# Kernel tuning notes

Hardware: AMD Instinct MI355X
Metric: run time of the kernel (lower is better)

Reference implementation:

```python
import jax, jax.numpy as jnp
import numpy as np

B, NQ, HW, C, H = 4, 1024, 4096, 1024, 8
DH = C // H  # 128


def setup_inputs() -> dict:
    key = jax.random.key(0)
    ks = jax.random.split(key, 11)
    s = 0.02
    return {
        "query": jax.random.normal(ks[0], (B, NQ, C), dtype=jnp.float32),
        "memory": jax.random.normal(ks[1], (B, HW, C), dtype=jnp.float32),
        "mask": jax.random.uniform(ks[2], (B, NQ, HW), dtype=jnp.float32),
        "Wq": jax.random.normal(ks[3], (C, C), dtype=jnp.float32) * s,
        "bq": jnp.zeros((C,), dtype=jnp.float32),
        "Wk": jax.random.normal(ks[4], (C, C), dtype=jnp.float32) * s,
        "bk": jnp.zeros((C,), dtype=jnp.float32),
        "Wv": jax.random.normal(ks[5], (C, C), dtype=jnp.float32) * s,
        "bv": jnp.zeros((C,), dtype=jnp.float32),
        "Wo": jax.random.normal(ks[6], (C, C), dtype=jnp.float32) * s,
        "bo": jnp.zeros((C,), dtype=jnp.float32),
    }


def reference(query, memory, mask, Wq, bq, Wk, bk, Wv, bv, Wo, bo):
    # Projections (torch nn.Linear convention: x @ W.T + b)
    q = (query @ Wq.T + bq).reshape(B, NQ, H, DH)
    k = (memory @ Wk.T + bk).reshape(B, HW, H, DH)
    v = (memory @ Wv.T + bv).reshape(B, HW, H, DH)

    scale = 1.0 / jnp.sqrt(jnp.asarray(DH, dtype=q.dtype))
    scores = jnp.einsum("bqhd,bkhd->bhqk", q * scale, k)  # [B,H,NQ,HW]

    # mask < 0.5 means disallowed (True in torch bool attn_mask -> -inf)
    allowed = (mask >= 0.5)[:, None, :, :]  # broadcast over heads
    scores = jnp.where(allowed, scores, jnp.asarray(-jnp.inf, dtype=scores.dtype))

    attn = jax.nn.softmax(scores, axis=-1)
    out = jnp.einsum("bhqk,bkhd->bqhd", attn, v).reshape(B, NQ, C)
    return out @ Wo.T + bo
```

## Files before the change

### kernel.cpp

```cpp
#include <hip/hip_runtime.h>


#define NB 4
#define NQL 1024
#define HWK 4096
#define CC 1024
#define NH 8
#define DHD 128

typedef __attribute__((ext_vector_type(8))) short s16x8;
typedef __attribute__((ext_vector_type(4))) short s16x4;
typedef __attribute__((ext_vector_type(4))) float f32x4;
typedef unsigned int u32;
typedef unsigned long long u64;
typedef const __attribute__((address_space(1))) u32* gas1;
typedef __attribute__((address_space(3))) u32* las3;

__device__ __forceinline__ unsigned short f2bf(float f) {
  u32 u = __float_as_uint(f);
  u32 r = u + 0x7FFFu + ((u >> 16) & 1u);
  return (unsigned short)(r >> 16);
}

__device__ __forceinline__ void gld16(const void* g, void* l) {
  __builtin_amdgcn_global_load_lds((gas1)g, (las3)l, 16, 0, 0);
}

#define MFMA16(a, b, c) __builtin_amdgcn_mfma_f32_16x16x32_bf16((a), (b), (c), 0, 0, 0)

__global__ void cvt_bf16(const float* __restrict__ s, short* __restrict__ d, int n8) {
  int i = blockIdx.x * 256 + threadIdx.x;
  int stride = gridDim.x * 256;
  for (; i < n8; i += stride) {
    const float4* s4 = (const float4*)s;
    float4 a = s4[i * 2];
    float4 b = s4[i * 2 + 1];
    s16x8 o;
    o[0] = (short)f2bf(a.x); o[1] = (short)f2bf(a.y);
    o[2] = (short)f2bf(a.z); o[3] = (short)f2bf(a.w);
    o[4] = (short)f2bf(b.x); o[5] = (short)f2bf(b.y);
    o[6] = (short)f2bf(b.z); o[7] = (short)f2bf(b.w);
    *(s16x8*)(d + (size_t)i * 8) = o;
  }
}

__global__ void mask_bits(const float* __restrict__ mask, u64* __restrict__ words) {
  int t = blockIdx.x * 256 + threadIdx.x;
  int wi = t >> 6;
  int lane = t & 63;
  int k = ((lane >> 2) & 3) * 16 + (lane >> 4) * 4 + (lane & 3);
  float v = mask[(size_t)wi * 64 + k];
  u64 bits = __ballot(v >= 0.5f);
  if (lane == 0) words[wi] = bits;
}

template <int EPI>
__global__ __launch_bounds__(256, 2) void gemm_bt(const short* __restrict__ A,
                                                  const short* __restrict__ W,
                                                  const float* __restrict__ bias,
                                                  void* __restrict__ Cout, float scale) {
  __shared__ alignas(16) short As[128 * 32];
  __shared__ alignas(16) short Bs[128 * 32];
  int nwg = gridDim.x;
  int bid = blockIdx.x;
  int wg = (bid & 7) * (nwg >> 3) + (bid >> 3);
  int bm = wg >> 3;
  int bn = wg & 7;
  int tid = threadIdx.x;
  int w = tid >> 6, lane = tid & 63, lo = lane & 15, hi = lane >> 4;
  int wr = w >> 1, wc = w & 1;
  const short* Ab = A + (size_t)bm * 128 * 1024;
  const short* Wb = W + (size_t)bn * 128 * 1024;
  f32x4 acc[4][4] = {};
  int srow = lane >> 2;
  int scolb = (lane & 3) * 16;

  for (int kt = 0; kt < 32; ++kt) {
    __syncthreads();
#pragma unroll
    for (int i = 0; i < 2; ++i) {
      int c = w * 2 + i;
      int row = c * 16 + srow;
      int sc = scolb ^ ((row & 3) << 4);
      gld16(Ab + (size_t)row * 1024 + kt * 32 + (sc >> 1), (char*)As + c * 1024);
      gld16(Wb + (size_t)row * 1024 + kt * 32 + (sc >> 1), (char*)Bs + c * 1024);
    }
    __syncthreads();
    s16x8 af[4], bf[4];
#pragma unroll
    for (int mf = 0; mf < 4; ++mf) {
      int row = wr * 64 + mf * 16 + lo;
      af[mf] = *(const s16x8*)((const char*)As + row * 64 + ((hi * 16) ^ ((row & 3) << 4)));
    }
#pragma unroll
    for (int nf = 0; nf < 4; ++nf) {
      int row = wc * 64 + nf * 16 + lo;
      bf[nf] = *(const s16x8*)((const char*)Bs + row * 64 + ((hi * 16) ^ ((row & 3) << 4)));
    }
#pragma unroll
    for (int mf = 0; mf < 4; ++mf)
#pragma unroll
      for (int nf = 0; nf < 4; ++nf) acc[mf][nf] = MFMA16(af[mf], bf[nf], acc[mf][nf]);
  }

#pragma unroll
  for (int nf = 0; nf < 4; ++nf) {
    int n = bn * 128 + wc * 64 + nf * 16 + lo;
    float bv = bias[n];
#pragma unroll
    for (int mf = 0; mf < 4; ++mf) {
      int m0 = bm * 128 + wr * 64 + mf * 16 + hi * 4;
      if constexpr (EPI == 0 || EPI == 1) {
        short* O = (short*)Cout;
#pragma unroll
        for (int r = 0; r < 4; ++r) {
          float v = acc[mf][nf][r] + bv;
          if constexpr (EPI == 0) v *= scale;
          O[(size_t)(m0 + r) * 1024 + n] = (short)f2bf(v);
        }
      } else if constexpr (EPI == 2) {
        short* O = (short*)Cout;
        int bb = m0 >> 12;
        int kk = m0 & 4095;
        s16x4 pk;
#pragma unroll
        for (int r = 0; r < 4; ++r) pk[r] = (short)f2bf(acc[mf][nf][r] + bv);
        *(s16x4*)(O + (size_t)bb * 4194304 + (size_t)n * 4096 + kk) = pk;
      } else {
        float* O = (float*)Cout;
#pragma unroll
        for (int r = 0; r < 4; ++r) O[(size_t)(m0 + r) * 1024 + n] = acc[mf][nf][r] + bv;
      }
    }
  }
}

__global__ __launch_bounds__(256, 2) void attn_kernel(const short* __restrict__ Qp,
                                                      const short* __restrict__ Kp,
                                                      const short* __restrict__ VT,
                                                      const u64* __restrict__ Mb,
                                                      short* __restrict__ AO) {
  __shared__ alignas(16) short Ks[2][8192];
  __shared__ alignas(16) short Vs[2][8192];
  __shared__ alignas(16) short Ps[4][1024];

  int bid = blockIdx.x;
  int wg = (bid & 7) * 64 + (bid >> 3);
  int bh = wg >> 4, qb = wg & 15;
  int b = bh >> 3, h = bh & 7;
  int tid = threadIdx.x, w = tid >> 6, lane = tid & 63, lo = lane & 15, hi = lane >> 4;
  int q0 = qb * 64 + w * 16;
  int q = q0 + lo;

  s16x8 qfr[4];
#pragma unroll
  for (int kf = 0; kf < 4; ++kf)
    qfr[kf] = *(const s16x8*)(Qp + (size_t)(b * NQL + q) * CC + h * DHD + kf * 32 + hi * 8);

  f32x4 acc[8] = {};
  float m_ = -3e38f;
  float l_ = 0.f;

  int krow = lane >> 4;
  int kcolb = (lane & 15) * 16;
  int vrow = lane >> 3;
  int vcolb = (lane & 7) * 16;

  auto stage = [&](int t, int buf) {
    int kv0 = t * 64;
#pragma unroll
    for (int i = 0; i < 4; ++i) {
      int c = w * 4 + i;
      int row = c * 4 + krow;
      int sc = kcolb ^ ((row & 7) << 4);
      gld16(Kp + (size_t)(b * HWK + kv0 + row) * CC + h * DHD + (sc >> 1), (char*)Ks[buf] + c * 1024);
    }
#pragma unroll
    for (int i = 0; i < 4; ++i) {
      int c = w * 4 + i;
      int d = c * 8 + vrow;
      int sc = vcolb ^ ((d & 7) << 4);
      gld16(VT + (size_t)((b * NH + h) * DHD + d) * HWK + kv0 + (sc >> 1), (char*)Vs[buf] + c * 1024);
    }
  };

  stage(0, 0);
  __syncthreads();

  for (int t = 0; t < 64; ++t) {
    int buf = t & 1;
    if (t < 63) stage(t + 1, buf ^ 1);

    __builtin_amdgcn_s_setprio(1);
    f32x4 st[4] = {};
#pragma unroll
    for (int nf = 0; nf < 4; ++nf) {
      int kidx = nf * 16 + lo;
      int swz = (kidx & 7) << 4;
#pragma unroll
      for (int kf = 0; kf < 4; ++kf) {
        s16x8 a = *(const s16x8*)((const char*)Ks[buf] + kidx * 256 + ((kf * 64 + hi * 16) ^ swz));
        st[nf] = MFMA16(a, qfr[kf], st[nf]);
      }
    }
    __builtin_amdgcn_s_setprio(0);

    u64 word = Mb[(size_t)(b * NQL + q) * 64 + t];
    u32 halfm = (u32)(word >> (hi * 16)) & 0xFFFFu;
    float smax = -3e38f;
#pragma unroll
    for (int nf = 0; nf < 4; ++nf)
#pragma unroll
      for (int r = 0; r < 4; ++r) smax = fmaxf(smax, st[nf][r]);
    smax = fmaxf(smax, __shfl_xor(smax, 16));
    smax = fmaxf(smax, __shfl_xor(smax, 32));

    if (__any(smax > m_ + 8.f)) {
      float mnew = fmaxf(m_, smax);
      float alpha = __builtin_amdgcn_exp2f(m_ - mnew);
      l_ *= alpha;
      m_ = mnew;
      float ar0 = __shfl(alpha, hi * 4 + 0);
      float ar1 = __shfl(alpha, hi * 4 + 1);
      float ar2 = __shfl(alpha, hi * 4 + 2);
      float ar3 = __shfl(alpha, hi * 4 + 3);
#pragma unroll
      for (int df = 0; df < 8; ++df) {
        acc[df][0] *= ar0; acc[df][1] *= ar1;
        acc[df][2] *= ar2; acc[df][3] *= ar3;
      }
    }

    float tsum = 0.f;
#pragma unroll
    for (int nf = 0; nf < 4; ++nf) {
      float p0 = __builtin_amdgcn_exp2f(st[nf][0] - m_);
      float p1 = __builtin_amdgcn_exp2f(st[nf][1] - m_);
      float p2 = __builtin_amdgcn_exp2f(st[nf][2] - m_);
      float p3 = __builtin_amdgcn_exp2f(st[nf][3] - m_);
      p0 = ((halfm >> (nf * 4 + 0)) & 1) ? p0 : 0.f;
      p1 = ((halfm >> (nf * 4 + 1)) & 1) ? p1 : 0.f;
      p2 = ((halfm >> (nf * 4 + 2)) & 1) ? p2 : 0.f;
      p3 = ((halfm >> (nf * 4 + 3)) & 1) ? p3 : 0.f;
      tsum += p0 + p1 + p2 + p3;
      u32 w0 = __builtin_amdgcn_perm(__float_as_uint(p1), __float_as_uint(p0), 0x07060302u);
      u32 w1 = __builtin_amdgcn_perm(__float_as_uint(p3), __float_as_uint(p2), 0x07060302u);
      uint2 pv; pv.x = w0; pv.y = w1;
      *(uint2*)((char*)Ps[w] + lo * 128 + ((nf * 32 + hi * 8) ^ ((lo & 7) << 4))) = pv;
    }
    tsum += __shfl_xor(tsum, 16);
    tsum += __shfl_xor(tsum, 32);
    l_ += tsum;
    asm volatile("" ::: "memory");

    __builtin_amdgcn_s_setprio(1);
#pragma unroll
    for (int kt = 0; kt < 2; ++kt) {
      s16x8 pa = *(const s16x8*)((const char*)Ps[w] + lo * 128 + ((kt * 64 + hi * 16) ^ ((lo & 7) << 4)));
#pragma unroll
      for (int df = 0; df < 8; ++df) {
        int d = df * 16 + lo;
        s16x8 vb = *(const s16x8*)((const char*)Vs[buf] + d * 128 + ((kt * 64 + hi * 16) ^ ((lo & 7) << 4)));
        acc[df] = MFMA16(pa, vb, acc[df]);
      }
    }
    __builtin_amdgcn_s_setprio(0);
    __syncthreads();
  }

  float linv = 1.0f / l_;
  float lr0 = __shfl(linv, hi * 4 + 0);
  float lr1 = __shfl(linv, hi * 4 + 1);
  float lr2 = __shfl(linv, hi * 4 + 2);
  float lr3 = __shfl(linv, hi * 4 + 3);
  int qbase = q0 + hi * 4;
#pragma unroll
  for (int df = 0; df < 8; ++df) {
    int col = h * DHD + df * 16 + lo;
    AO[(size_t)(b * NQL + qbase + 0) * CC + col] = (short)f2bf(acc[df][0] * lr0);
    AO[(size_t)(b * NQL + qbase + 1) * CC + col] = (short)f2bf(acc[df][1] * lr1);
    AO[(size_t)(b * NQL + qbase + 2) * CC + col] = (short)f2bf(acc[df][2] * lr2);
    AO[(size_t)(b * NQL + qbase + 3) * CC + col] = (short)f2bf(acc[df][3] * lr3);
  }
}

extern "C" void kernel_launch(void* const* d_in, const int* in_sizes, int n_in,
                              void* d_out, int out_size, void* d_ws, size_t ws_size,
                              hipStream_t stream) {
  (void)in_sizes; (void)n_in; (void)out_size; (void)ws_size;
  const float* query = (const float*)d_in[0];
  const float* memory = (const float*)d_in[1];
  const float* mask = (const float*)d_in[2];
  const float* Wq = (const float*)d_in[3];
  const float* bq = (const float*)d_in[4];
  const float* Wk = (const float*)d_in[5];
  const float* bk = (const float*)d_in[6];
  const float* Wv = (const float*)d_in[7];
  const float* bv = (const float*)d_in[8];
  const float* Wo = (const float*)d_in[9];
  const float* bo = (const float*)d_in[10];
  float* out = (float*)d_out;

  char* ws = (char*)d_ws;
  short* qbf = (short*)(ws);
  short* mbf = (short*)(ws + (8ull << 20));
  short* wqb = (short*)(ws + (40ull << 20));
  short* wkb = wqb + (1u << 20);
  short* wvb = wqb + (2u << 20);
  short* wob = wqb + (3u << 20);
  u64* mbits = (u64*)(ws + (48ull << 20));
  short* Qp = (short*)(ws + (50ull << 20));
  short* Kp = (short*)(ws + (58ull << 20));
  short* VT = (short*)(ws + (90ull << 20));
  short* AO = (short*)(ws + (122ull << 20));

  cvt_bf16<<<2048, 256, 0, stream>>>(query, qbf, (NB * NQL * CC) / 8);
  cvt_bf16<<<2048, 256, 0, stream>>>(memory, mbf, (NB * HWK * CC) / 8);
  cvt_bf16<<<512, 256, 0, stream>>>(Wq, wqb, (CC * CC) / 8);
  cvt_bf16<<<512, 256, 0, stream>>>(Wk, wkb, (CC * CC) / 8);
  cvt_bf16<<<512, 256, 0, stream>>>(Wv, wvb, (CC * CC) / 8);
  cvt_bf16<<<512, 256, 0, stream>>>(Wo, wob, (CC * CC) / 8);
  mask_bits<<<65536, 256, 0, stream>>>(mask, mbits);

  const float qscale = 0.08838834764831845f * 1.4426950408889634f;
  gemm_bt<0><<<256, 256, 0, stream>>>(qbf, wqb, bq, Qp, qscale);
  gemm_bt<1><<<1024, 256, 0, stream>>>(mbf, wkb, bk, Kp, 1.0f);
  gemm_bt<2><<<1024, 256, 0, stream>>>(mbf, wvb, bv, VT, 1.0f);
  attn_kernel<<<512, 256, 0, stream>>>(Qp, Kp, VT, mbits, AO);
  gemm_bt<3><<<256, 256, 0, stream>>>(AO, wob, bo, out, 1.0f);
}
```

Before: 459.4 us.

## Double-buffer GEMM tiles, merge weight casts, relayout mask bits, hoist attention addresses

Several changes land together. The projection GEMM gets double-buffered shared-memory tiles with one barrier per k-step and precomputed source pointers, and its launch bound rises to 3 blocks per CU. The four weight conversions become one launch, and mask_bits becomes a grid-stride kernel that writes the bit words in a [b][qblock][t][q] layout with a simple bit order. The attention kernel precomputes its K/V/mask pointers and issues the mask word load before the stage loads so it overlaps, and decodes mask bits to match the new layout. Doubling the GEMM LDS and raising occupancy may limit registers.

```diff
diff --git a/kernel.cpp b/kernel.cpp
--- a/kernel.cpp
+++ b/kernel.cpp
@@ -44,23 +44,46 @@
   }
 }
 
+__global__ void cvt_w4(const float* s0, const float* s1, const float* s2, const float* s3,
+                       short* d0, short* d1, short* d2, short* d3) {
+  int bb = blockIdx.x;
+  int si = bb >> 9;
+  const float* s = si == 0 ? s0 : si == 1 ? s1 : si == 2 ? s2 : s3;
+  short* d = si == 0 ? d0 : si == 1 ? d1 : si == 2 ? d2 : d3;
+  int i = (bb & 511) * 256 + threadIdx.x;
+  const float4* s4 = (const float4*)s;
+  float4 a = s4[i * 2];
+  float4 b = s4[i * 2 + 1];
+  s16x8 o;
+  o[0] = (short)f2bf(a.x); o[1] = (short)f2bf(a.y);
+  o[2] = (short)f2bf(a.z); o[3] = (short)f2bf(a.w);
+  o[4] = (short)f2bf(b.x); o[5] = (short)f2bf(b.y);
+  o[6] = (short)f2bf(b.z); o[7] = (short)f2bf(b.w);
+  *(s16x8*)(d + (size_t)i * 8) = o;
+}
+
 __global__ void mask_bits(const float* __restrict__ mask, u64* __restrict__ words) {
-  int t = blockIdx.x * 256 + threadIdx.x;
-  int wi = t >> 6;
-  int lane = t & 63;
-  int k = ((lane >> 2) & 3) * 16 + (lane >> 4) * 4 + (lane & 3);
-  float v = mask[(size_t)wi * 64 + k];
-  u64 bits = __ballot(v >= 0.5f);
-  if (lane == 0) words[wi] = bits;
+  int gw = (blockIdx.x * 256 + threadIdx.x) >> 6;
+  int lane = threadIdx.x & 63;
+  int nw = (gridDim.x * 256) >> 6;
+  for (int wi = gw; wi < 262144; wi += nw) {
+    int ql = wi & 63;
+    int t = (wi >> 6) & 63;
+    int qh = (wi >> 12) & 15;
+    int bb = wi >> 16;
+    size_t src = ((size_t)((bb << 10) + (qh << 6) + ql) << 12) + t * 64 + lane;
+    u64 bits = __ballot(mask[src] >= 0.5f);
+    if (lane == 0) words[wi] = bits;
+  }
 }
 
 template <int EPI>
-__global__ __launch_bounds__(256, 2) void gemm_bt(const short* __restrict__ A,
+__global__ __launch_bounds__(256, 3) void gemm_bt(const short* __restrict__ A,
                                                   const short* __restrict__ W,
                                                   const float* __restrict__ bias,
                                                   void* __restrict__ Cout, float scale) {
-  __shared__ alignas(16) short As[128 * 32];
-  __shared__ alignas(16) short Bs[128 * 32];
+  __shared__ alignas(16) short As[2][4096];
+  __shared__ alignas(16) short Bs[2][4096];
   int nwg = gridDim.x;
   int bid = blockIdx.x;
   int wg = (bid & 7) * (nwg >> 3) + (bid >> 3);
@@ -75,32 +98,48 @@
   int srow = lane >> 2;
   int scolb = (lane & 3) * 16;
 
-  for (int kt = 0; kt < 32; ++kt) {
-    __syncthreads();
+  const short* asrc[2];
+  const short* bsrc[2];
+#pragma unroll
+  for (int i = 0; i < 2; ++i) {
+    int c = w * 2 + i;
+    int row = c * 16 + srow;
+    int sc = scolb ^ ((row & 3) << 4);
+    asrc[i] = Ab + (size_t)row * 1024 + (sc >> 1);
+    bsrc[i] = Wb + (size_t)row * 1024 + (sc >> 1);
+  }
+
+  auto stage = [&](int kt, int bufi) {
 #pragma unroll
     for (int i = 0; i < 2; ++i) {
       int c = w * 2 + i;
-      int row = c * 16 + srow;
-      int sc = scolb ^ ((row & 3) << 4);
-      gld16(Ab + (size_t)row * 1024 + kt * 32 + (sc >> 1), (char*)As + c * 1024);
-      gld16(Wb + (size_t)row * 1024 + kt * 32 + (sc >> 1), (char*)Bs + c * 1024);
-    }
-    __syncthreads();
+      gld16(asrc[i] + kt * 32, (char*)As[bufi] + c * 1024);
+      gld16(bsrc[i] + kt * 32, (char*)Bs[bufi] + c * 1024);
+    }
+  };
+
+  stage(0, 0);
+  __syncthreads();
+  int buf = 0;
+  for (int kt = 0; kt < 32; ++kt) {
+    if (kt < 31) stage(kt + 1, buf ^ 1);
     s16x8 af[4], bf[4];
 #pragma unroll
     for (int mf = 0; mf < 4; ++mf) {
       int row = wr * 64 + mf * 16 + lo;
-      af[mf] = *(const s16x8*)((const char*)As + row * 64 + ((hi * 16) ^ ((row & 3) << 4)));
+      af[mf] = *(const s16x8*)((const char*)As[buf] + row * 64 + ((hi * 16) ^ ((row & 3) << 4)));
     }
 #pragma unroll
     for (int nf = 0; nf < 4; ++nf) {
       int row = wc * 64 + nf * 16 + lo;
-      bf[nf] = *(const s16x8*)((const char*)Bs + row * 64 + ((hi * 16) ^ ((row & 3) << 4)));
+      bf[nf] = *(const s16x8*)((const char*)Bs[buf] + row * 64 + ((hi * 16) ^ ((row & 3) << 4)));
     }
 #pragma unroll
     for (int mf = 0; mf < 4; ++mf)
 #pragma unroll
       for (int nf = 0; nf < 4; ++nf) acc[mf][nf] = MFMA16(af[mf], bf[nf], acc[mf][nf]);
+    __syncthreads();
+    buf ^= 1;
   }
 
 #pragma unroll
@@ -166,22 +205,27 @@
   int vrow = lane >> 3;
   int vcolb = (lane & 7) * 16;
 
-  auto stage = [&](int t, int buf) {
-    int kv0 = t * 64;
-#pragma unroll
-    for (int i = 0; i < 4; ++i) {
-      int c = w * 4 + i;
-      int row = c * 4 + krow;
-      int sc = kcolb ^ ((row & 7) << 4);
-      gld16(Kp + (size_t)(b * HWK + kv0 + row) * CC + h * DHD + (sc >> 1), (char*)Ks[buf] + c * 1024);
-    }
-#pragma unroll
-    for (int i = 0; i < 4; ++i) {
-      int c = w * 4 + i;
-      int d = c * 8 + vrow;
-      int sc = vcolb ^ ((d & 7) << 4);
-      gld16(VT + (size_t)((b * NH + h) * DHD + d) * HWK + kv0 + (sc >> 1), (char*)Vs[buf] + c * 1024);
-    }
+  const short* kbase[4];
+  const short* vbase[4];
+#pragma unroll
+  for (int i = 0; i < 4; ++i) {
+    int c = w * 4 + i;
+    int row = c * 4 + krow;
+    int sc = kcolb ^ ((row & 7) << 4);
+    kbase[i] = Kp + (size_t)(b * HWK + row) * CC + h * DHD + (sc >> 1);
+    int d = c * 8 + vrow;
+    int scv = vcolb ^ ((d & 7) << 4);
+    vbase[i] = VT + (size_t)((b * NH + h) * DHD + d) * HWK + (scv >> 1);
+  }
+  const u64* mp = Mb + ((size_t)(b * 16 + qb) << 12) + (w * 16 + lo);
+
+  auto stage = [&](int t, int bufi) {
+#pragma unroll
+    for (int i = 0; i < 4; ++i)
+      gld16(kbase[i] + ((size_t)t << 16), (char*)Ks[bufi] + (w * 4 + i) * 1024);
+#pragma unroll
+    for (int i = 0; i < 4; ++i)
+      gld16(vbase[i] + ((size_t)t << 6), (char*)Vs[bufi] + (w * 4 + i) * 1024);
   };
 
   stage(0, 0);
@@ -189,6 +233,7 @@
 
   for (int t = 0; t < 64; ++t) {
     int buf = t & 1;
+    u64 word = mp[(size_t)t << 6];
     if (t < 63) stage(t + 1, buf ^ 1);
 
     __builtin_amdgcn_s_setprio(1);
@@ -205,8 +250,8 @@
     }
     __builtin_amdgcn_s_setprio(0);
 
-    u64 word = Mb[(size_t)(b * NQL + q) * 64 + t];
-    u32 halfm = (u32)(word >> (hi * 16)) & 0xFFFFu;
+    u64 sh = word >> (hi * 4);
+    u32 mlo32 = (u32)sh, mhi32 = (u32)(sh >> 32);
     float smax = -3e38f;
 #pragma unroll
     for (int nf = 0; nf < 4; ++nf)
@@ -234,14 +279,16 @@
     float tsum = 0.f;
 #pragma unroll
     for (int nf = 0; nf < 4; ++nf) {
+      u32 mx = (nf < 2) ? mlo32 : mhi32;
+      int bs = (nf & 1) * 16;
       float p0 = __builtin_amdgcn_exp2f(st[nf][0] - m_);
       float p1 = __builtin_amdgcn_exp2f(st[nf][1] - m_);
       float p2 = __builtin_amdgcn_exp2f(st[nf][2] - m_);
       float p3 = __builtin_amdgcn_exp2f(st[nf][3] - m_);
-      p0 = ((halfm >> (nf * 4 + 0)) & 1) ? p0 : 0.f;
-      p1 = ((halfm >> (nf * 4 + 1)) & 1) ? p1 : 0.f;
-      p2 = ((halfm >> (nf * 4 + 2)) & 1) ? p2 : 0.f;
-      p3 = ((halfm >> (nf * 4 + 3)) & 1) ? p3 : 0.f;
+      p0 = ((mx >> (bs + 0)) & 1) ? p0 : 0.f;
+      p1 = ((mx >> (bs + 1)) & 1) ? p1 : 0.f;
+      p2 = ((mx >> (bs + 2)) & 1) ? p2 : 0.f;
+      p3 = ((mx >> (bs + 3)) & 1) ? p3 : 0.f;
       tsum += p0 + p1 + p2 + p3;
       u32 w0 = __builtin_amdgcn_perm(__float_as_uint(p1), __float_as_uint(p0), 0x07060302u);
       u32 w1 = __builtin_amdgcn_perm(__float_as_uint(p3), __float_as_uint(p2), 0x07060302u);
@@ -316,11 +363,8 @@
 
   cvt_bf16<<<2048, 256, 0, stream>>>(query, qbf, (NB * NQL * CC) / 8);
   cvt_bf16<<<2048, 256, 0, stream>>>(memory, mbf, (NB * HWK * CC) / 8);
-  cvt_bf16<<<512, 256, 0, stream>>>(Wq, wqb, (CC * CC) / 8);
-  cvt_bf16<<<512, 256, 0, stream>>>(Wk, wkb, (CC * CC) / 8);
-  cvt_bf16<<<512, 256, 0, stream>>>(Wv, wvb, (CC * CC) / 8);
-  cvt_bf16<<<512, 256, 0, stream>>>(Wo, wob, (CC * CC) / 8);
-  mask_bits<<<65536, 256, 0, stream>>>(mask, mbits);
+  cvt_w4<<<2048, 256, 0, stream>>>(Wq, Wk, Wv, Wo, wqb, wkb, wvb, wob);
+  mask_bits<<<4096, 256, 0, stream>>>(mask, mbits);
 
   const float qscale = 0.08838834764831845f * 1.4426950408889634f;
   gemm_bt<0><<<256, 256, 0, stream>>>(qbf, wqb, bq, Qp, qscale);
```

After: 451.9 us. No clear change (-1.6%).
